# Performance work log

Hardware: AMD Instinct MI355X
Metric: run time of the kernel (lower is better)

Reference implementation:

```python
import jax, jax.numpy as jnp
import numpy as np

N = 50000      # nodes
E = 400000     # edges per hop
IN = 256       # in_channels
H = 4          # heads
C = 64         # out_channels per head
NEG = 0.2      # leaky relu negative slope


def setup_inputs() -> dict:
    key = jax.random.key(0)
    ks = jax.random.split(key, 10)
    x = jax.random.normal(ks[0], (N, IN), dtype=jnp.float32)
    edge_index1 = jax.random.randint(ks[1], (2, E), 0, N, dtype=jnp.int32)
    edge_index2 = jax.random.randint(ks[2], (2, E), 0, N, dtype=jnp.int32)
    s = 0.05
    Wl0 = jax.random.normal(ks[3], (IN, H * C), dtype=jnp.float32) * s
    Wr0 = jax.random.normal(ks[4], (IN, H * C), dtype=jnp.float32) * s
    att0 = jax.random.normal(ks[5], (H, C), dtype=jnp.float32) * s
    Wl1 = jax.random.normal(ks[6], (IN, H * C), dtype=jnp.float32) * s
    Wr1 = jax.random.normal(ks[7], (IN, H * C), dtype=jnp.float32) * s
    att1 = jax.random.normal(ks[8], (H, C), dtype=jnp.float32) * s
    return {"x": x, "Wl0": Wl0, "Wr0": Wr0, "att0": att0,
            "Wl1": Wl1, "Wr1": Wr1, "att1": att1,
            "edge_index1": edge_index1, "edge_index2": edge_index2}


def _gatv2_hop(x, Wl, Wr, att, src, dst):
    """One GATv2Conv hop (bias=False, residual=False, eval-mode dropout, concat=False)."""
    n = x.shape[0]
    xl = (x @ Wl).reshape(n, H, C)   # source-side projection
    xr = (x @ Wr).reshape(n, H, C)   # target-side projection
    # edge-wise GATv2 score: a^T leaky_relu(x_l[j] + x_r[i])
    m = jax.nn.leaky_relu(xl[src] + xr[dst], NEG)            # [E, H, C]
    e = jnp.einsum('ehc,hc->eh', m, att)                     # [E, H]
    # segment softmax over incoming edges of each destination node
    e_max = jax.lax.stop_gradient(
        jax.ops.segment_max(e, dst, num_segments=n))         # [N, H]
    ex = jnp.exp(e - e_max[dst])
    denom = jax.ops.segment_sum(ex, dst, num_segments=n)     # [N, H]
    alpha = ex / (denom[dst] + 1e-16)                        # [E, H]
    msg = xl[src] * alpha[:, :, None]                        # [E, H, C]
    out = jax.ops.segment_sum(msg, dst, num_segments=n)      # [N, H, C]
    return out.mean(axis=1)                                  # concat=False -> mean heads


def reference(x, Wl0, Wr0, att0, Wl1, Wr1, att1, edge_index1, edge_index2):
    n = x.shape[0]
    # hop 0: add_self_loops=True
    loop = jnp.arange(n, dtype=edge_index1.dtype)
    src0 = jnp.concatenate([edge_index1[0], loop])
    dst0 = jnp.concatenate([edge_index1[1], loop])
    out = _gatv2_hop(x, Wl0, Wr0, att0, src0, dst0)
    # hop 1: no self loops, scaled by 1/(k+1) = 1/2
    out = out + _gatv2_hop(x, Wl1, Wr1, att1, edge_index2[0], edge_index2[1]) / 2.0
    return out
```

## Files before the change

### kernel.cpp

```cpp
#include <hip/hip_runtime.h>

typedef unsigned int uint;
typedef unsigned short ushort;

typedef __bf16 bf16x8 __attribute__((ext_vector_type(8)));
typedef float f32x4 __attribute__((ext_vector_type(4)));

#define CAP 48
#define RSTR 136

__device__ __forceinline__ float bf2f(ushort u) {
    return __uint_as_float(((uint)u) << 16);
}
__device__ __forceinline__ ushort f2bf(float f) {
    uint u = __float_as_uint(f);
    u += 0x7fffu + ((u >> 16) & 1u);
    return (ushort)(u >> 16);
}
__device__ __forceinline__ float4 up4(ushort4 v) {
    return make_float4(bf2f(v.x), bf2f(v.y), bf2f(v.z), bf2f(v.w));
}
__device__ __forceinline__ void load_lds16(const ushort* g, ushort* l) {
    __builtin_amdgcn_global_load_lds(
        (const __attribute__((address_space(1))) void*)g,
        (__attribute__((address_space(3))) void*)l, 16, 0, 0);
}
__device__ __forceinline__ int swz(int row) { return (row + (row >> 2)) & 3; }
__device__ __forceinline__ ushort4 gload(const ushort* __restrict__ base, uint off) {
    return *(const ushort4*)((const char*)base + off);
}

__global__ __launch_bounds__(256) void prep(
    const float* __restrict__ X, ushort* __restrict__ Xb, int Nrows, int Mpad,
    const float* __restrict__ Wl0, const float* __restrict__ Wr0,
    const float* __restrict__ Wl1, const float* __restrict__ Wr1,
    ushort* __restrict__ Wt,
    int* __restrict__ cnt0, int* __restrict__ cnt1)
{
    const int BX = Mpad / 8;
    int blk = blockIdx.x;
    if (blk < BX) {
        int i = blk * 256 + threadIdx.x;
        int base = i * 8;
        int row = base >> 8;
        ushort o[8];
        if (row < Nrows) {
            float4 v0 = *(const float4*)(X + base);
            float4 v1 = *(const float4*)(X + base + 4);
            o[0] = f2bf(v0.x); o[1] = f2bf(v0.y); o[2] = f2bf(v0.z); o[3] = f2bf(v0.w);
            o[4] = f2bf(v1.x); o[5] = f2bf(v1.y); o[6] = f2bf(v1.z); o[7] = f2bf(v1.w);
        } else {
#pragma unroll
            for (int j = 0; j < 8; j++) o[j] = 0;
        }
        *(uint4*)(Xb + base) = *(const uint4*)o;
        return;
    }
    blk -= BX;
    if (blk < 1024) {
        int n = blk;
        int k = threadIdx.x;
        const float* W = (n < 256) ? Wl0 : (n < 512) ? Wr0 : (n < 768) ? Wl1 : Wr1;
        Wt[n * 256 + k] = f2bf(W[k * 256 + (n & 255)]);
        return;
    }
    blk -= 1024;
    int d = blk * 256 + threadIdx.x;
    if (d < Nrows) {
        cnt0[d] = 0;
        cnt1[d] = 0;
    }
}

__global__ __launch_bounds__(256) void csr_scatter2(
    const int* __restrict__ ei1, const int* __restrict__ ei2,
    int* __restrict__ cnt0, int* __restrict__ srcs0,
    int* __restrict__ cnt1, int* __restrict__ srcs1,
    int E1, int E2)
{
    int e = blockIdx.x * 256 + threadIdx.x;
    if (e < E1) {
        int d = ei1[E1 + e];
        int pos = atomicAdd(&cnt0[d], 1);
        if (pos < CAP) srcs0[(size_t)d * CAP + pos] = ei1[e];
    } else if (e < E1 + E2) {
        int e2 = e - E1;
        int d = ei2[E2 + e2];
        int pos = atomicAdd(&cnt1[d], 1);
        if (pos < CAP) srcs1[(size_t)d * CAP + pos] = ei2[e2];
    }
}

__global__ __launch_bounds__(256, 2) void gemm_mfma(
    const ushort* __restrict__ Xb,
    const ushort* __restrict__ Wt,
    ushort* __restrict__ XP,
    int Nrows)
{
    __shared__ ushort SH[64 * RSTR];
    ushort* As = SH;
    ushort* Bs = SH + 128 * 32;

    const int tid = threadIdx.x;
    const int w = tid >> 6, l = tid & 63;
    const int wm = w & 1, wn = w >> 1;
    const int m0 = blockIdx.y * 128;
    const int n0g = blockIdx.x * 128;

    f32x4 acc[4][4];
#pragma unroll
    for (int i = 0; i < 4; i++)
#pragma unroll
        for (int j = 0; j < 4; j++) acc[i][j] = (f32x4)(0.f);

    const int fr = l & 15, fq = l >> 4;
    int a_off[4], b_off[4];
#pragma unroll
    for (int t = 0; t < 4; t++) {
        int rA = wm * 64 + t * 16 + fr;
        a_off[t] = (rA * 4 + ((fq + swz(rA)) & 3)) * 8;
        int rB = wn * 64 + t * 16 + fr;
        b_off[t] = (rB * 4 + ((fq + swz(rB)) & 3)) * 8;
    }

    for (int k0 = 0; k0 < 256; k0 += 32) {
        __syncthreads();
#pragma unroll
        for (int r = 0; r < 2; r++) {
            int slot = r * 256 + tid;
            int row = slot >> 2;
            int kp = ((slot & 3) - swz(row)) & 3;
            load_lds16(Xb + (size_t)(m0 + row) * 256 + k0 + kp * 8,
                       &As[(r * 256 + w * 64) * 8]);
            load_lds16(Wt + (size_t)(n0g + row) * 256 + k0 + kp * 8,
                       &Bs[(r * 256 + w * 64) * 8]);
        }
        __syncthreads();

        bf16x8 a[4], b[4];
#pragma unroll
        for (int t = 0; t < 4; t++) {
            a[t] = *(const bf16x8*)(As + a_off[t]);
            b[t] = *(const bf16x8*)(Bs + b_off[t]);
        }
#pragma unroll
        for (int mi = 0; mi < 4; mi++)
#pragma unroll
            for (int ni = 0; ni < 4; ni++)
                acc[mi][ni] = __builtin_amdgcn_mfma_f32_16x16x32_bf16(
                    a[mi], b[ni], acc[mi][ni], 0, 0, 0);
    }

    ushort* OUT = XP + (size_t)(n0g >> 8) * ((size_t)Nrows * 256);
    const int colbase = n0g & 255;
    const int cb = wn * 64 + fr;
#pragma unroll
    for (int r = 0; r < 2; r++) {
        __syncthreads();
#pragma unroll
        for (int mm = 0; mm < 2; mm++) {
            int mi = 2 * r + mm;
            int brb = (wm * 32 + mm * 16 + fq * 4) * RSTR + cb;
#pragma unroll
            for (int reg = 0; reg < 4; reg++)
#pragma unroll
                for (int ni = 0; ni < 4; ni++)
                    SH[brb + reg * RSTR + ni * 16] = f2bf(acc[mi][ni][reg]);
        }
        __syncthreads();
        int br = tid >> 2;
        int grow = m0 + (br >> 5) * 64 + (2 * r + ((br >> 4) & 1)) * 16 + (br & 15);
        bool ok = (grow < Nrows);
        int cc = (tid & 3) * 8;
#pragma unroll
        for (int q = 0; q < 4; q++) {
            uint4 v = *(const uint4*)(SH + br * RSTR + cc + q * 32);
            if (ok) *(uint4*)(OUT + (size_t)grow * 256 + colbase + cc + q * 32) = v;
        }
    }
}

__device__ __forceinline__ void eacc(ushort4 raw, bool live,
    const float4& xr, const float4& av,
    float& a0, float& a1, float& a2, float& a3, float& den)
{
    float x0 = bf2f(raw.x), x1 = bf2f(raw.y), x2 = bf2f(raw.z), x3 = bf2f(raw.w);
    float t0 = x0 + xr.x, t1 = x1 + xr.y, t2 = x2 + xr.z, t3 = x3 + xr.w;
    float m0 = fmaxf(t0, 0.2f * t0), m1 = fmaxf(t1, 0.2f * t1);
    float m2 = fmaxf(t2, 0.2f * t2), m3 = fmaxf(t3, 0.2f * t3);
    float p = av.x * m0;
    p = fmaf(av.y, m1, p);
    p = fmaf(av.z, m2, p);
    p = fmaf(av.w, m3, p);
    p += __shfl_xor(p, 1);
    p += __shfl_xor(p, 2);
    p += __shfl_xor(p, 4);
    p += __shfl_xor(p, 8);
    float pe = __expf(p);
    if (!live) pe = 0.f;
    den += pe;
    a0 = fmaf(pe, x0, a0);
    a1 = fmaf(pe, x1, a1);
    a2 = fmaf(pe, x2, a2);
    a3 = fmaf(pe, x3, a3);
}

__device__ __forceinline__ void gat_hop(
    const ushort* __restrict__ XL, const ushort* __restrict__ XR,
    const float* __restrict__ att, const int* __restrict__ cnt,
    const int* __restrict__ srcs, int self, int d, int lane, uint lo8,
    float& o0, float& o1, float& o2, float& o3)
{
    float4 xr = up4(gload(XR, (uint)d * 512 + lo8));
    float4 av = *(const float4*)(att + lane * 4);

    int m = __builtin_amdgcn_readfirstlane(cnt[d]);
    if (m > CAP) m = CAP;
    const int c = (m > 0) ? (m - 1) : 0;
    int slot = (lane < m) ? lane : c;
    int sv = srcs[(size_t)d * CAP + slot];

    float a0 = 0.f, a1 = 0.f, a2 = 0.f, a3 = 0.f, den = 0.f;

    if (self) {
        eacc(gload(XL, (uint)d * 512 + lo8), true, xr, av, a0, a1, a2, a3, den);
    }
    if (m > 0) {
        ushort4 pf[4];
#pragma unroll
        for (int j = 0; j < 4; j++) {
            int jj = (j < c) ? j : c;
            uint s = (uint)__builtin_amdgcn_readlane(sv, jj);
            pf[j] = gload(XL, s * 512 + lo8);
        }
        for (int i = 0; i < m; i += 4) {
            ushort4 c0 = pf[0], c1 = pf[1], c2 = pf[2], c3 = pf[3];
            int b = i + 4;
            if (b <= c) {
#pragma unroll
                for (int j = 0; j < 4; j++) {
                    int t = b + j;
                    int jj = (t < c) ? t : c;
                    uint s = (uint)__builtin_amdgcn_readlane(sv, jj);
                    pf[j] = gload(XL, s * 512 + lo8);
                }
            }
            eacc(c0, true,      xr, av, a0, a1, a2, a3, den);
            eacc(c1, i + 1 < m, xr, av, a0, a1, a2, a3, den);
            eacc(c2, i + 2 < m, xr, av, a0, a1, a2, a3, den);
            eacc(c3, i + 3 < m, xr, av, a0, a1, a2, a3, den);
        }
    }
    float inv = 1.f / (den + 1e-16f);
    o0 = a0 * inv; o1 = a1 * inv; o2 = a2 * inv; o3 = a3 * inv;
}

__global__ __launch_bounds__(256) void gat_fused(
    const ushort* __restrict__ XL0, const ushort* __restrict__ XR0,
    const float* __restrict__ att0,
    const int* __restrict__ cnt0, const int* __restrict__ srcs0,
    int self0, float scale0,
    const ushort* __restrict__ XL1, const ushort* __restrict__ XR1,
    const float* __restrict__ att1,
    const int* __restrict__ cnt1, const int* __restrict__ srcs1,
    float scale1,
    const float* __restrict__ base, float* __restrict__ outp, int N)
{
    int d = blockIdx.x * 4 + (threadIdx.x >> 6);
    if (d >= N) return;
    int lane = threadIdx.x & 63;
    uint lo8 = (uint)lane * 8;

    float r0, r1, r2, r3;
    gat_hop(XL0, XR0, att0, cnt0, srcs0, self0, d, lane, lo8, r0, r1, r2, r3);
    float v0 = scale0 * r0, v1 = scale0 * r1, v2 = scale0 * r2, v3 = scale0 * r3;
    if (cnt1) {
        float s0, s1, s2, s3;
        gat_hop(XL1, XR1, att1, cnt1, srcs1, 0, d, lane, lo8, s0, s1, s2, s3);
        v0 = fmaf(scale1, s0, v0); v1 = fmaf(scale1, s1, v1);
        v2 = fmaf(scale1, s2, v2); v3 = fmaf(scale1, s3, v3);
    }
    v0 += __shfl_xor(v0, 16); v0 += __shfl_xor(v0, 32);
    v1 += __shfl_xor(v1, 16); v1 += __shfl_xor(v1, 32);
    v2 += __shfl_xor(v2, 16); v2 += __shfl_xor(v2, 32);
    v3 += __shfl_xor(v3, 16); v3 += __shfl_xor(v3, 32);
    int jsel = lane >> 4;
    float vv = (jsel == 0) ? v0 : (jsel == 1) ? v1 : (jsel == 2) ? v2 : v3;
    int ch = ((lane & 15) << 2) + jsel;
    float prev = base ? base[(size_t)d * 64 + ch] : 0.f;
    outp[(size_t)d * 64 + ch] = prev + vv;
}

extern "C" void kernel_launch(void* const* d_in, const int* in_sizes, int n_in,
                              void* d_out, int out_size, void* d_ws, size_t ws_size,
                              hipStream_t stream)
{
    const float* x    = (const float*)d_in[0];
    const float* Wl0  = (const float*)d_in[1];
    const float* Wr0  = (const float*)d_in[2];
    const float* att0 = (const float*)d_in[3];
    const float* Wl1  = (const float*)d_in[4];
    const float* Wr1  = (const float*)d_in[5];
    const float* att1 = (const float*)d_in[6];
    const int* ei1 = (const int*)d_in[7];
    const int* ei2 = (const int*)d_in[8];

    const int N  = in_sizes[0] / 256;
    const int E1 = in_sizes[7] / 2;
    const int E2 = in_sizes[8] / 2;
    const int Mpad = ((N + 127) / 128) * 128;
    const size_t NB = (size_t)N * 256;

    char* ws = (char*)d_ws;
    size_t off = 0;
    ushort* Xb  = (ushort*)(ws + off); off += (size_t)Mpad * 256 * sizeof(ushort);
    ushort* Wt  = (ushort*)(ws + off); off += (size_t)1024 * 256 * sizeof(ushort);
    int* cnt0   = (int*)(ws + off);    off += (size_t)N * sizeof(int);
    int* cnt1   = (int*)(ws + off);    off += (size_t)N * sizeof(int);
    int* srcs0  = (int*)(ws + off);    off += (size_t)N * CAP * sizeof(int);
    int* srcs1  = (int*)(ws + off);    off += (size_t)N * CAP * sizeof(int);
    ushort* XP  = (ushort*)(ws + off);
    size_t need_mega = off + 4 * NB * sizeof(ushort);
    const bool mega = (ws_size >= need_mega);
    float* outf = (float*)d_out;

    const int BX = Mpad / 8;
    int prep_blocks = BX + 1024 + (N + 255) / 256;
    prep<<<prep_blocks, 256, 0, stream>>>(x, Xb, N, Mpad, Wl0, Wr0, Wl1, Wr1,
                                          Wt, cnt0, cnt1);
    csr_scatter2<<<(E1 + E2 + 255) / 256, 256, 0, stream>>>(
        ei1, ei2, cnt0, srcs0, cnt1, srcs1, E1, E2);

    int aggblk = (N + 3) / 4;
    if (mega) {
        gemm_mfma<<<dim3(8, Mpad / 128), 256, 0, stream>>>(Xb, Wt, XP, N);
        gat_fused<<<aggblk, 256, 0, stream>>>(
            XP, XP + NB, att0, cnt0, srcs0, 1, 0.25f,
            XP + 2 * NB, XP + 3 * NB, att1, cnt1, srcs1, 0.125f,
            nullptr, outf, N);
    } else {
        gemm_mfma<<<dim3(4, Mpad / 128), 256, 0, stream>>>(Xb, Wt, XP, N);
        gat_fused<<<aggblk, 256, 0, stream>>>(
            XP, XP + NB, att0, cnt0, srcs0, 1, 0.25f,
            nullptr, nullptr, nullptr, nullptr, nullptr, 0.f,
            nullptr, outf, N);
        gemm_mfma<<<dim3(4, Mpad / 128), 256, 0, stream>>>(Xb, Wt + 512 * 256, XP, N);
        gat_fused<<<aggblk, 256, 0, stream>>>(
            XP, XP + NB, att1, cnt1, srcs1, 0, 0.125f,
            nullptr, nullptr, nullptr, nullptr, nullptr, 0.f,
            outf, outf, N);
    }
}
```

Measured before the change: 272.8 us.

## Fuse CSR scatter into prep kernel and use packed-float math in aggregation

The edge-scatter kernel is merged into the prep kernel, and the counter zeroing moves to a hipMemsetAsync so the scatter blocks can run in the same launch as the bf16 conversion and weight transpose. This removes one kernel launch and its dependency gap. The GAT edge accumulation is rewritten with 2-wide float vectors so the compiler can emit packed FP32 instructions, and it uses two interleaved accumulator sets to shorten the dependency chain. It adds a memset call and changes the order of floating-point summation.

After: 289.8 us. 1.06x slower.

```diff
diff --git a/kernel.cpp b/kernel.cpp
--- a/kernel.cpp
+++ b/kernel.cpp
@@ -5,6 +5,7 @@
 
 typedef __bf16 bf16x8 __attribute__((ext_vector_type(8)));
 typedef float f32x4 __attribute__((ext_vector_type(4)));
+typedef float f32x2 __attribute__((ext_vector_type(2)));
 
 #define CAP 48
 #define RSTR 136
@@ -17,17 +18,14 @@
     u += 0x7fffu + ((u >> 16) & 1u);
     return (ushort)(u >> 16);
 }
-__device__ __forceinline__ float4 up4(ushort4 v) {
-    return make_float4(bf2f(v.x), bf2f(v.y), bf2f(v.z), bf2f(v.w));
-}
 __device__ __forceinline__ void load_lds16(const ushort* g, ushort* l) {
     __builtin_amdgcn_global_load_lds(
         (const __attribute__((address_space(1))) void*)g,
         (__attribute__((address_space(3))) void*)l, 16, 0, 0);
 }
 __device__ __forceinline__ int swz(int row) { return (row + (row >> 2)) & 3; }
-__device__ __forceinline__ ushort4 gload(const ushort* __restrict__ base, uint off) {
-    return *(const ushort4*)((const char*)base + off);
+__device__ __forceinline__ uint2 gload2(const ushort* __restrict__ base, uint off) {
+    return *(const uint2*)((const char*)base + off);
 }
 
 __global__ __launch_bounds__(256) void prep(
@@ -35,7 +33,10 @@
     const float* __restrict__ Wl0, const float* __restrict__ Wr0,
     const float* __restrict__ Wl1, const float* __restrict__ Wr1,
     ushort* __restrict__ Wt,
-    int* __restrict__ cnt0, int* __restrict__ cnt1)
+    const int* __restrict__ ei1, const int* __restrict__ ei2,
+    int* __restrict__ cnt0, int* __restrict__ srcs0,
+    int* __restrict__ cnt1, int* __restrict__ srcs1,
+    int E1, int E2)
 {
     const int BX = Mpad / 8;
     int blk = blockIdx.x;
@@ -65,20 +66,7 @@
         return;
     }
     blk -= 1024;
-    int d = blk * 256 + threadIdx.x;
-    if (d < Nrows) {
-        cnt0[d] = 0;
-        cnt1[d] = 0;
-    }
-}
-
-__global__ __launch_bounds__(256) void csr_scatter2(
-    const int* __restrict__ ei1, const int* __restrict__ ei2,
-    int* __restrict__ cnt0, int* __restrict__ srcs0,
-    int* __restrict__ cnt1, int* __restrict__ srcs1,
-    int E1, int E2)
-{
-    int e = blockIdx.x * 256 + threadIdx.x;
+    int e = blk * 256 + threadIdx.x;
     if (e < E1) {
         int d = ei1[E1 + e];
         int pos = atomicAdd(&cnt0[d], 1);
@@ -180,18 +168,21 @@
     }
 }
 
-__device__ __forceinline__ void eacc(ushort4 raw, bool live,
-    const float4& xr, const float4& av,
-    float& a0, float& a1, float& a2, float& a3, float& den)
-{
-    float x0 = bf2f(raw.x), x1 = bf2f(raw.y), x2 = bf2f(raw.z), x3 = bf2f(raw.w);
-    float t0 = x0 + xr.x, t1 = x1 + xr.y, t2 = x2 + xr.z, t3 = x3 + xr.w;
-    float m0 = fmaxf(t0, 0.2f * t0), m1 = fmaxf(t1, 0.2f * t1);
-    float m2 = fmaxf(t2, 0.2f * t2), m3 = fmaxf(t3, 0.2f * t3);
-    float p = av.x * m0;
-    p = fmaf(av.y, m1, p);
-    p = fmaf(av.z, m2, p);
-    p = fmaf(av.w, m3, p);
+__device__ __forceinline__ void eacc2(uint2 raw, bool live,
+    const f32x2& xr01, const f32x2& xr23, const f32x2& av01, const f32x2& av23,
+    f32x2& a01, f32x2& a23, float& den)
+{
+    f32x2 x01, x23;
+    x01[0] = __uint_as_float(raw.x << 16);
+    x01[1] = __uint_as_float(raw.x & 0xffff0000u);
+    x23[0] = __uint_as_float(raw.y << 16);
+    x23[1] = __uint_as_float(raw.y & 0xffff0000u);
+    f32x2 t01 = x01 + xr01;
+    f32x2 t23 = x23 + xr23;
+    f32x2 l01 = __builtin_elementwise_max(t01, 0.2f * t01);
+    f32x2 l23 = __builtin_elementwise_max(t23, 0.2f * t23);
+    f32x2 dd = av01 * l01 + av23 * l23;
+    float p = dd[0] + dd[1];
     p += __shfl_xor(p, 1);
     p += __shfl_xor(p, 2);
     p += __shfl_xor(p, 4);
@@ -199,10 +190,8 @@
     float pe = __expf(p);
     if (!live) pe = 0.f;
     den += pe;
-    a0 = fmaf(pe, x0, a0);
-    a1 = fmaf(pe, x1, a1);
-    a2 = fmaf(pe, x2, a2);
-    a3 = fmaf(pe, x3, a3);
+    a01 += x01 * pe;
+    a23 += x23 * pe;
 }
 
 __device__ __forceinline__ void gat_hop(
@@ -211,8 +200,14 @@
     const int* __restrict__ srcs, int self, int d, int lane, uint lo8,
     float& o0, float& o1, float& o2, float& o3)
 {
-    float4 xr = up4(gload(XR, (uint)d * 512 + lo8));
+    uint2 xrr = gload2(XR, (uint)d * 512 + lo8);
+    f32x2 xr01, xr23;
+    xr01[0] = __uint_as_float(xrr.x << 16);
+    xr01[1] = __uint_as_float(xrr.x & 0xffff0000u);
+    xr23[0] = __uint_as_float(xrr.y << 16);
+    xr23[1] = __uint_as_float(xrr.y & 0xffff0000u);
     float4 av = *(const float4*)(att + lane * 4);
+    f32x2 av01 = {av.x, av.y}, av23 = {av.z, av.w};
 
     int m = __builtin_amdgcn_readfirstlane(cnt[d]);
     if (m > CAP) m = CAP;
@@ -220,21 +215,24 @@
     int slot = (lane < m) ? lane : c;
     int sv = srcs[(size_t)d * CAP + slot];
 
-    float a0 = 0.f, a1 = 0.f, a2 = 0.f, a3 = 0.f, den = 0.f;
+    f32x2 a01a = (f32x2)0.f, a23a = (f32x2)0.f;
+    f32x2 a01b = (f32x2)0.f, a23b = (f32x2)0.f;
+    float dena = 0.f, denb = 0.f;
 
     if (self) {
-        eacc(gload(XL, (uint)d * 512 + lo8), true, xr, av, a0, a1, a2, a3, den);
+        eacc2(gload2(XL, (uint)d * 512 + lo8), true,
+              xr01, xr23, av01, av23, a01a, a23a, dena);
     }
     if (m > 0) {
-        ushort4 pf[4];
+        uint2 pf[4];
 #pragma unroll
         for (int j = 0; j < 4; j++) {
             int jj = (j < c) ? j : c;
             uint s = (uint)__builtin_amdgcn_readlane(sv, jj);
-            pf[j] = gload(XL, s * 512 + lo8);
+            pf[j] = gload2(XL, s * 512 + lo8);
         }
         for (int i = 0; i < m; i += 4) {
-            ushort4 c0 = pf[0], c1 = pf[1], c2 = pf[2], c3 = pf[3];
+            uint2 c0 = pf[0], c1 = pf[1], c2 = pf[2], c3 = pf[3];
             int b = i + 4;
             if (b <= c) {
 #pragma unroll
@@ -242,17 +240,18 @@
                     int t = b + j;
                     int jj = (t < c) ? t : c;
                     uint s = (uint)__builtin_amdgcn_readlane(sv, jj);
-                    pf[j] = gload(XL, s * 512 + lo8);
+                    pf[j] = gload2(XL, s * 512 + lo8);
                 }
             }
-            eacc(c0, true,      xr, av, a0, a1, a2, a3, den);
-            eacc(c1, i + 1 < m, xr, av, a0, a1, a2, a3, den);
-            eacc(c2, i + 2 < m, xr, av, a0, a1, a2, a3, den);
-            eacc(c3, i + 3 < m, xr, av, a0, a1, a2, a3, den);
-        }
-    }
-    float inv = 1.f / (den + 1e-16f);
-    o0 = a0 * inv; o1 = a1 * inv; o2 = a2 * inv; o3 = a3 * inv;
+            eacc2(c0, true,      xr01, xr23, av01, av23, a01a, a23a, dena);
+            eacc2(c1, i + 1 < m, xr01, xr23, av01, av23, a01b, a23b, denb);
+            eacc2(c2, i + 2 < m, xr01, xr23, av01, av23, a01a, a23a, dena);
+            eacc2(c3, i + 3 < m, xr01, xr23, av01, av23, a01b, a23b, denb);
+        }
+    }
+    f32x2 a01 = a01a + a01b, a23 = a23a + a23b;
+    float inv = 1.f / (dena + denb + 1e-16f);
+    o0 = a01[0] * inv; o1 = a01[1] * inv; o2 = a23[0] * inv; o3 = a23[1] * inv;
 }
 
 __global__ __launch_bounds__(256) void gat_fused(
@@ -324,11 +323,12 @@
     const bool mega = (ws_size >= need_mega);
     float* outf = (float*)d_out;
 
+    hipMemsetAsync(cnt0, 0, 2 * (size_t)N * sizeof(int), stream);
+
     const int BX = Mpad / 8;
-    int prep_blocks = BX + 1024 + (N + 255) / 256;
-    prep<<<prep_blocks, 256, 0, stream>>>(x, Xb, N, Mpad, Wl0, Wr0, Wl1, Wr1,
-                                          Wt, cnt0, cnt1);
-    csr_scatter2<<<(E1 + E2 + 255) / 256, 256, 0, stream>>>(
+    const int SB = (E1 + E2 + 255) / 256;
+    prep<<<BX + 1024 + SB, 256, 0, stream>>>(
+        x, Xb, N, Mpad, Wl0, Wr0, Wl1, Wr1, Wt,
         ei1, ei2, cnt0, srcs0, cnt1, srcs1, E1, E2);
 
     int aggblk = (N + 3) / 4;
```

## Process two edges per wavefront with 16-byte loads and DPP head reductions

Applied to the files above, without the earlier changes.

Each wavefront now splits into two 32-lane halves that each handle a different source edge, and every lane loads 16 bytes (8 bf16 channels) of the source row instead of 8. The per-head dot-product reduction switches from four shuffles to three DPP adds, the self loop is folded into the edge list, and the softmax denominator is combined across halves before normalisation. The aim is to halve loop iterations and the shuffle overhead, and to issue wider gathers. The cost is more registers per lane (8 accumulators plus 8 xr values) and extra cross-half shuffles in the epilogue.

Result: no change. 272.7 us (-0.0%).

```diff
diff --git a/kernel.cpp b/kernel.cpp
--- a/kernel.cpp
+++ b/kernel.cpp
@@ -17,17 +17,17 @@
     u += 0x7fffu + ((u >> 16) & 1u);
     return (ushort)(u >> 16);
 }
-__device__ __forceinline__ float4 up4(ushort4 v) {
-    return make_float4(bf2f(v.x), bf2f(v.y), bf2f(v.z), bf2f(v.w));
-}
 __device__ __forceinline__ void load_lds16(const ushort* g, ushort* l) {
     __builtin_amdgcn_global_load_lds(
         (const __attribute__((address_space(1))) void*)g,
         (__attribute__((address_space(3))) void*)l, 16, 0, 0);
 }
 __device__ __forceinline__ int swz(int row) { return (row + (row >> 2)) & 3; }
-__device__ __forceinline__ ushort4 gload(const ushort* __restrict__ base, uint off) {
-    return *(const ushort4*)((const char*)base + off);
+
+template<int CTRL>
+__device__ __forceinline__ float dppadd(float p) {
+    int t = __builtin_amdgcn_update_dpp(0, __float_as_int(p), CTRL, 0xf, 0xf, true);
+    return p + __int_as_float(t);
 }
 
 __global__ __launch_bounds__(256) void prep(
@@ -180,79 +180,102 @@
     }
 }
 
-__device__ __forceinline__ void eacc(ushort4 raw, bool live,
-    const float4& xr, const float4& av,
-    float& a0, float& a1, float& a2, float& a3, float& den)
-{
-    float x0 = bf2f(raw.x), x1 = bf2f(raw.y), x2 = bf2f(raw.z), x3 = bf2f(raw.w);
-    float t0 = x0 + xr.x, t1 = x1 + xr.y, t2 = x2 + xr.z, t3 = x3 + xr.w;
-    float m0 = fmaxf(t0, 0.2f * t0), m1 = fmaxf(t1, 0.2f * t1);
-    float m2 = fmaxf(t2, 0.2f * t2), m3 = fmaxf(t3, 0.2f * t3);
-    float p = av.x * m0;
-    p = fmaf(av.y, m1, p);
-    p = fmaf(av.z, m2, p);
-    p = fmaf(av.w, m3, p);
-    p += __shfl_xor(p, 1);
-    p += __shfl_xor(p, 2);
-    p += __shfl_xor(p, 4);
-    p += __shfl_xor(p, 8);
+
+__device__ __forceinline__ uint4 pair_load(const ushort* __restrict__ XL, int sv,
+                                           int e, int cp, uint hl, uint sub16)
+{
+    int eA = (e     < cp) ? e     : cp;
+    int eB = (e + 1 < cp) ? e + 1 : cp;
+    uint sA = (uint)__builtin_amdgcn_readlane(sv, eA) * 512u;
+    uint sB = (uint)__builtin_amdgcn_readlane(sv, eB) * 512u;
+    uint off = sA + hl * (sB - sA) + sub16;
+    return *(const uint4*)((const char*)XL + off);
+}
+
+__device__ __forceinline__ void eaccp(uint4 raw, int deadB, uint hl,
+    const float* __restrict__ xr8, const float* __restrict__ av,
+    float* __restrict__ acc, float& den)
+{
+    float x[8];
+    x[0] = __uint_as_float(raw.x << 16);
+    x[1] = __uint_as_float(raw.x & 0xffff0000u);
+    x[2] = __uint_as_float(raw.y << 16);
+    x[3] = __uint_as_float(raw.y & 0xffff0000u);
+    x[4] = __uint_as_float(raw.z << 16);
+    x[5] = __uint_as_float(raw.z & 0xffff0000u);
+    x[6] = __uint_as_float(raw.w << 16);
+    x[7] = __uint_as_float(raw.w & 0xffff0000u);
+    float p0 = 0.f, p1 = 0.f;
+#pragma unroll
+    for (int j = 0; j < 4; j++) {
+        float t = x[j] + xr8[j];
+        float lr = fmaxf(t, 0.2f * t);
+        p0 = fmaf(av[j], lr, p0);
+    }
+#pragma unroll
+    for (int j = 4; j < 8; j++) {
+        float t = x[j] + xr8[j];
+        float lr = fmaxf(t, 0.2f * t);
+        p1 = fmaf(av[j], lr, p1);
+    }
+    float p = p0 + p1;
+    p = dppadd<0xB1>(p);
+    p = dppadd<0x4E>(p);
+    p = dppadd<0x141>(p);
     float pe = __expf(p);
-    if (!live) pe = 0.f;
+    if (deadB & (int)hl) pe = 0.f;
     den += pe;
-    a0 = fmaf(pe, x0, a0);
-    a1 = fmaf(pe, x1, a1);
-    a2 = fmaf(pe, x2, a2);
-    a3 = fmaf(pe, x3, a3);
+#pragma unroll
+    for (int j = 0; j < 8; j++) acc[j] = fmaf(pe, x[j], acc[j]);
 }
 
 __device__ __forceinline__ void gat_hop(
     const ushort* __restrict__ XL, const ushort* __restrict__ XR,
     const float* __restrict__ att, const int* __restrict__ cnt,
-    const int* __restrict__ srcs, int self, int d, int lane, uint lo8,
-    float& o0, float& o1, float& o2, float& o3)
-{
-    float4 xr = up4(gload(XR, (uint)d * 512 + lo8));
-    float4 av = *(const float4*)(att + lane * 4);
+    const int* __restrict__ srcs, int self, int d, int lane,
+    uint hl, uint sub, uint sub16,
+    float* __restrict__ acc, float& den)
+{
+    uint4 xrr = *(const uint4*)((const char*)XR + (uint)d * 512u + sub16);
+    float xr8[8];
+    xr8[0] = __uint_as_float(xrr.x << 16);
+    xr8[1] = __uint_as_float(xrr.x & 0xffff0000u);
+    xr8[2] = __uint_as_float(xrr.y << 16);
+    xr8[3] = __uint_as_float(xrr.y & 0xffff0000u);
+    xr8[4] = __uint_as_float(xrr.z << 16);
+    xr8[5] = __uint_as_float(xrr.z & 0xffff0000u);
+    xr8[6] = __uint_as_float(xrr.w << 16);
+    xr8[7] = __uint_as_float(xrr.w & 0xffff0000u);
+    float av[8];
+    *(float4*)(av)     = *(const float4*)(att + sub * 8);
+    *(float4*)(av + 4) = *(const float4*)(att + sub * 8 + 4);
+
+#pragma unroll
+    for (int j = 0; j < 8; j++) acc[j] = 0.f;
+    den = 0.f;
 
     int m = __builtin_amdgcn_readfirstlane(cnt[d]);
     if (m > CAP) m = CAP;
-    const int c = (m > 0) ? (m - 1) : 0;
-    int slot = (lane < m) ? lane : c;
+    const int mt = m + self;
+    if (mt <= 0) return;
+
+    int idx = lane - self;
+    int mm1 = (m > 0) ? (m - 1) : 0;
+    int slot = idx < 0 ? 0 : (idx > mm1 ? mm1 : idx);
     int sv = srcs[(size_t)d * CAP + slot];
-
-    float a0 = 0.f, a1 = 0.f, a2 = 0.f, a3 = 0.f, den = 0.f;
-
-    if (self) {
-        eacc(gload(XL, (uint)d * 512 + lo8), true, xr, av, a0, a1, a2, a3, den);
-    }
-    if (m > 0) {
-        ushort4 pf[4];
-#pragma unroll
-        for (int j = 0; j < 4; j++) {
-            int jj = (j < c) ? j : c;
-            uint s = (uint)__builtin_amdgcn_readlane(sv, jj);
-            pf[j] = gload(XL, s * 512 + lo8);
-        }
-        for (int i = 0; i < m; i += 4) {
-            ushort4 c0 = pf[0], c1 = pf[1], c2 = pf[2], c3 = pf[3];
-            int b = i + 4;
-            if (b <= c) {
-#pragma unroll
-                for (int j = 0; j < 4; j++) {
-                    int t = b + j;
-                    int jj = (t < c) ? t : c;
-                    uint s = (uint)__builtin_amdgcn_readlane(sv, jj);
-                    pf[j] = gload(XL, s * 512 + lo8);
-                }
-            }
-            eacc(c0, true,      xr, av, a0, a1, a2, a3, den);
-            eacc(c1, i + 1 < m, xr, av, a0, a1, a2, a3, den);
-            eacc(c2, i + 2 < m, xr, av, a0, a1, a2, a3, den);
-            eacc(c3, i + 3 < m, xr, av, a0, a1, a2, a3, den);
-        }
-    }
-    float inv = 1.f / (den + 1e-16f);
-    o0 = a0 * inv; o1 = a1 * inv; o2 = a2 * inv; o3 = a3 * inv;
+    if (self && lane == 0) sv = d;
+
+    const int cp = mt - 1;
+    uint4 pf0 = pair_load(XL, sv, 0, cp, hl, sub16);
+    uint4 pf1 = pair_load(XL, sv, 2, cp, hl, sub16);
+    for (int i = 0; i < mt; i += 4) {
+        uint4 c0 = pf0, c1 = pf1;
+        pf0 = pair_load(XL, sv, i + 4, cp, hl, sub16);
+        pf1 = pair_load(XL, sv, i + 6, cp, hl, sub16);
+        eaccp(c0, (i + 1 >= mt) ? 1 : 0, hl, xr8, av, acc, den);
+        if (i + 2 < mt)
+            eaccp(c1, (i + 3 >= mt) ? 1 : 0, hl, xr8, av, acc, den);
+    }
 }
 
 __global__ __launch_bounds__(256) void gat_fused(
@@ -269,26 +292,46 @@
     int d = blockIdx.x * 4 + (threadIdx.x >> 6);
     if (d >= N) return;
     int lane = threadIdx.x & 63;
-    uint lo8 = (uint)lane * 8;
-
-    float r0, r1, r2, r3;
-    gat_hop(XL0, XR0, att0, cnt0, srcs0, self0, d, lane, lo8, r0, r1, r2, r3);
-    float v0 = scale0 * r0, v1 = scale0 * r1, v2 = scale0 * r2, v3 = scale0 * r3;
+    uint hl = (uint)(lane >> 5);
+    uint sub = (uint)(lane & 31);
+    uint sub16 = sub * 16u;
+
+    float acc0[8], den0;
+    gat_hop(XL0, XR0, att0, cnt0, srcs0, self0, d, lane, hl, sub, sub16, acc0, den0);
+
+    float v[8];
+    den0 += __shfl_xor(den0, 32);
+    float s0 = scale0 / (den0 + 1e-16f);
     if (cnt1) {
-        float s0, s1, s2, s3;
-        gat_hop(XL1, XR1, att1, cnt1, srcs1, 0, d, lane, lo8, s0, s1, s2, s3);
-        v0 = fmaf(scale1, s0, v0); v1 = fmaf(scale1, s1, v1);
-        v2 = fmaf(scale1, s2, v2); v3 = fmaf(scale1, s3, v3);
-    }
-    v0 += __shfl_xor(v0, 16); v0 += __shfl_xor(v0, 32);
-    v1 += __shfl_xor(v1, 16); v1 += __shfl_xor(v1, 32);
-    v2 += __shfl_xor(v2, 16); v2 += __shfl_xor(v2, 32);
-    v3 += __shfl_xor(v3, 16); v3 += __shfl_xor(v3, 32);
-    int jsel = lane >> 4;
-    float vv = (jsel == 0) ? v0 : (jsel == 1) ? v1 : (jsel == 2) ? v2 : v3;
-    int ch = ((lane & 15) << 2) + jsel;
-    float prev = base ? base[(size_t)d * 64 + ch] : 0.f;
-    outp[(size_t)d * 64 + ch] = prev + vv;
+        float acc1[8], den1;
+        gat_hop(XL1, XR1, att1, cnt1, srcs1, 0, d, lane, hl, sub, sub16, acc1, den1);
+        den1 += __shfl_xor(den1, 32);
+        float s1 = scale1 / (den1 + 1e-16f);
+#pragma unroll
+        for (int j = 0; j < 8; j++) v[j] = acc0[j] * s0 + acc1[j] * s1;
+    } else {
+#pragma unroll
+        for (int j = 0; j < 8; j++) v[j] = acc0[j] * s0;
+    }
+#pragma unroll
+    for (int j = 0; j < 8; j++) {
+        v[j] += __shfl_xor(v[j], 8);
+        v[j] += __shfl_xor(v[j], 16);
+        v[j] += __shfl_xor(v[j], 32);
+    }
+    if (lane < 8) {
+        float* dst = outp + (size_t)d * 64 + lane * 8;
+        float4 w0 = {v[0], v[1], v[2], v[3]};
+        float4 w1 = {v[4], v[5], v[6], v[7]};
+        if (base) {
+            float4 b0 = *(const float4*)(base + (size_t)d * 64 + lane * 8);
+            float4 b1 = *(const float4*)(base + (size_t)d * 64 + lane * 8 + 4);
+            w0.x += b0.x; w0.y += b0.y; w0.z += b0.z; w0.w += b0.w;
+            w1.x += b1.x; w1.y += b1.y; w1.z += b1.z; w1.w += b1.w;
+        }
+        *(float4*)dst = w0;
+        *(float4*)(dst + 4) = w1;
+    }
 }
 
 extern "C" void kernel_launch(void* const* d_in, const int* in_sizes, int n_in,
```
